# Optimization experiments

Hardware: AMD Instinct MI355X
Metric: run time of the kernel (lower is better)

Reference implementation:

```python
import jax, jax.numpy as jnp
import numpy as np
import math

B, S, D, H, DFF = 16, 512, 1024, 16, 4096
DK = D // H
EPS = 1e-6


def _lin(x, W, b):
    return x @ W + b


def _layernorm(x, g, b):
    # torch-style: unbiased std, eps added to std (not var)
    m = jnp.mean(x, axis=-1, keepdims=True)
    std = jnp.sqrt(jnp.sum((x - m) ** 2, axis=-1, keepdims=True) / (x.shape[-1] - 1))
    return g * (x - m) / (std + EPS) + b


def _gelu(x):
    return 0.5 * x * (1.0 + jnp.tanh(jnp.sqrt(2.0 / jnp.pi) * (x + 0.044715 * x ** 3)))


def setup_inputs() -> dict:
    key = jax.random.key(0)
    ks = jax.random.split(key, 20)
    sc = lambda fan_in: 1.0 / math.sqrt(fan_in)
    d = {
        "x": jax.random.normal(ks[0], (B, S, D), jnp.float32),
        "time": jax.random.normal(ks[1], (B, S, D), jnp.float32),
        "Wq": jax.random.uniform(ks[2], (D, D), jnp.float32, -sc(D), sc(D)),
        "bq": jnp.zeros((D,), jnp.float32),
        "Wk": jax.random.uniform(ks[3], (D, D), jnp.float32, -sc(D), sc(D)),
        "bk": jnp.zeros((D,), jnp.float32),
        "Wt": jax.random.uniform(ks[4], (D, D), jnp.float32, -sc(D), sc(D)),
        "bt": jnp.zeros((D,), jnp.float32),
        "Wv": jax.random.uniform(ks[5], (D, D), jnp.float32, -sc(D), sc(D)),
        "bv": jnp.zeros((D,), jnp.float32),
        "Wo": jax.random.uniform(ks[6], (D, D), jnp.float32, -sc(D), sc(D)),
        "bo": jnp.zeros((D,), jnp.float32),
        "W1": jax.random.uniform(ks[7], (D, DFF), jnp.float32, -sc(D), sc(D)),
        "b1": jnp.zeros((DFF,), jnp.float32),
        "W2": jax.random.uniform(ks[8], (DFF, D), jnp.float32, -sc(DFF), sc(DFF)),
        "b2": jnp.zeros((D,), jnp.float32),
        "ln1_g": jnp.ones((D,), jnp.float32),
        "ln1_b": jnp.zeros((D,), jnp.float32),
        "ln2_g": jnp.ones((D,), jnp.float32),
        "ln2_b": jnp.zeros((D,), jnp.float32),
        "mask_logits": jax.random.uniform(ks[9], (S, S), jnp.float32, 2.0, 5.0),
        "mask": jax.random.randint(ks[10], (B, 1, S, S), 0, 2, jnp.int32),
        "pmask": 0,
    }
    return d


def reference(x, time, Wq, bq, Wk, bk, Wt, bt, Wv, bv, Wo, bo, W1, b1, W2, b2,
              ln1_g, ln1_b, ln2_g, ln2_b, mask_logits, mask, pmask):
    def split_heads(t):  # [B,S,D] -> [B,H,S,DK]
        return t.reshape(B, S, H, DK).transpose(0, 2, 1, 3)

    # --- attention sublayer (dropout = identity at inference) ---
    xn = _layernorm(x, ln1_g, ln1_b)
    q = split_heads(_lin(xn, Wq, bq))
    k1 = split_heads(_lin(xn, Wk, bk))
    k2 = split_heads(_lin(time, Wt, bt))
    v = split_heads(_lin(xn, Wv, bv))

    inv = 1.0 / math.sqrt(DK)
    scores = jnp.einsum("bhqd,bhkd->bhqk", q, k1) * inv
    scores = jnp.where(mask == 0, -1e9, scores)  # masked_fill BEFORE time term
    scores = scores + jnp.einsum("bhqd,bhkd->bhqk", q, k2) * inv
    p_attn = jax.nn.softmax(scores, axis=-1)
    p_attn = p_attn * jax.nn.sigmoid(mask_logits)  # learned post-softmax mask [S,S]
    ctx = jnp.einsum("bhqk,bhkd->bhqd", p_attn, v)
    ctx = ctx.transpose(0, 2, 1, 3).reshape(B, S, D)
    x = x + _lin(ctx, Wo, bo)

    # --- FFN sublayer ---
    xn2 = _layernorm(x, ln2_g, ln2_b)
    ff = _lin(_gelu(_lin(xn2, W1, b1)), W2, b2)
    return x + ff
```

## Files before the change

### kernel.cpp

```cpp
#include <hip/hip_runtime.h>

#define BB   16
#define SS   512
#define DD   1024
#define HH   16
#define DKK  64
#define DFFN 4096
#define LN_EPS 1e-6f
#define QSCALE 0.18033688011112042f

typedef __attribute__((ext_vector_type(8))) __bf16 bf16x8;
typedef __attribute__((ext_vector_type(4))) float f32x4;
typedef __attribute__((ext_vector_type(8))) unsigned short ushort8;
typedef __attribute__((ext_vector_type(4))) unsigned short ushort4_t;

#define AS1 __attribute__((address_space(1)))
#define AS3 __attribute__((address_space(3)))

__device__ __forceinline__ unsigned short f2bf(float f) {
  unsigned int u = __float_as_uint(f);
  u += 0x7FFFu + ((u >> 16) & 1u);
  return (unsigned short)(u >> 16);
}
__device__ __forceinline__ float bf2f(unsigned short u) {
  return __uint_as_float(((unsigned int)u) << 16);
}

__device__ __forceinline__ float gelu_f(float x) {
  float x3 = x * x * x;
  return 0.5f * x * (1.0f + tanhf(0.7978845608028654f * (x + 0.044715f * x3)));
}

__device__ __forceinline__ void sbar() {
  __builtin_amdgcn_sched_barrier(0);
  __builtin_amdgcn_s_barrier();
  __builtin_amdgcn_sched_barrier(0);
}
#define WAITVM(N)                                         \
  do {                                                    \
    __builtin_amdgcn_sched_barrier(0);                    \
    asm volatile("s_waitcnt vmcnt(" #N ")" ::: "memory"); \
    __builtin_amdgcn_sched_barrier(0);                    \
  } while (0)

__global__ __launch_bounds__(256) void ln_kernel(const float* __restrict__ x,
                                                 const float* __restrict__ g,
                                                 const float* __restrict__ b,
                                                 unsigned short* __restrict__ out, int ldo) {
  const int row = blockIdx.x;
  const int tid = threadIdx.x;
  const float* xr = x + (size_t)row * DD;
  float4 v = *(const float4*)(xr + tid * 4);
  float s = v.x + v.y + v.z + v.w;
#pragma unroll
  for (int off = 1; off < 64; off <<= 1) s += __shfl_xor(s, off);
  __shared__ float red[8];
  const int wid = tid >> 6, l = tid & 63;
  if (l == 0) red[wid] = s;
  __syncthreads();
  const float mean = (red[0] + red[1] + red[2] + red[3]) * (1.0f / DD);
  float4 d;
  d.x = v.x - mean; d.y = v.y - mean; d.z = v.z - mean; d.w = v.w - mean;
  float ss = d.x * d.x + d.y * d.y + d.z * d.z + d.w * d.w;
#pragma unroll
  for (int off = 1; off < 64; off <<= 1) ss += __shfl_xor(ss, off);
  if (l == 0) red[4 + wid] = ss;
  __syncthreads();
  const float var = (red[4] + red[5] + red[6] + red[7]) * (1.0f / (DD - 1));
  const float scale = 1.0f / (sqrtf(var) + LN_EPS);
  float4 gv = *(const float4*)(g + tid * 4);
  float4 bv = *(const float4*)(b + tid * 4);
  ushort4_t o;
  o[0] = f2bf(gv.x * d.x * scale + bv.x);
  o[1] = f2bf(gv.y * d.y * scale + bv.y);
  o[2] = f2bf(gv.z * d.z * scale + bv.z);
  o[3] = f2bf(gv.w * d.w * scale + bv.w);
  *(ushort4_t*)(out + (size_t)row * ldo + tid * 4) = o;
}

__global__ __launch_bounds__(256) void cvt_bf16(const float* __restrict__ in,
                                                unsigned short* __restrict__ out, int ldo) {
  const int i = blockIdx.x * 256 + threadIdx.x;
  const int row = i >> 7;
  const int c0 = (i & 127) * 8;
  const float4* p = (const float4*)(in + (size_t)row * DD + c0);
  float4 a = p[0], b = p[1];
  ushort8 o;
  o[0] = f2bf(a.x); o[1] = f2bf(a.y); o[2] = f2bf(a.z); o[3] = f2bf(a.w);
  o[4] = f2bf(b.x); o[5] = f2bf(b.y); o[6] = f2bf(b.z); o[7] = f2bf(b.w);
  *(ushort8*)(out + (size_t)row * ldo + c0) = o;
}

__global__ __launch_bounds__(256) void transpose_cvt(const float* __restrict__ W,
                                                     unsigned short* __restrict__ WT,
                                                     int N, int ldo) {
  __shared__ float tile[32][33];
  const int tx = threadIdx.x & 31, ty = threadIdx.x >> 5;
  const int n0 = blockIdx.x * 32, k0 = blockIdx.y * 32;
#pragma unroll
  for (int i = 0; i < 32; i += 8)
    tile[ty + i][tx] = W[(size_t)(k0 + ty + i) * N + n0 + tx];
  __syncthreads();
#pragma unroll
  for (int i = 0; i < 32; i += 8)
    WT[(size_t)(n0 + ty + i) * ldo + k0 + tx] = f2bf(tile[tx][ty + i]);
}

__global__ __launch_bounds__(256) void vtrans(const unsigned short* __restrict__ in,
                                              unsigned short* __restrict__ out) {
  __shared__ unsigned short tile[64][72];
  const int t = threadIdx.x;
  const int c0 = blockIdx.x * 64;
  const int r0 = blockIdx.y * 64;
  const int tx = t & 15, ty = t >> 4;
#pragma unroll
  for (int i = 0; i < 64; i += 16)
    *(ushort4_t*)&tile[ty + i][tx * 4] =
        *(const ushort4_t*)(in + (size_t)(r0 + ty + i) * 1024 + c0 + tx * 4);
  __syncthreads();
  const int cT = t >> 2, rq = (t & 3) * 16;
  ushort8 o0, o1;
#pragma unroll
  for (int j = 0; j < 8; ++j) o0[j] = tile[rq + j][cT];
#pragma unroll
  for (int j = 0; j < 8; ++j) o1[j] = tile[rq + 8 + j][cT];
  *(ushort8*)(out + (size_t)(c0 + cT) * 8192 + r0 + rq) = o0;
  *(ushort8*)(out + (size_t)(c0 + cT) * 8192 + r0 + rq + 8) = o1;
}

__global__ __launch_bounds__(256) void bias_prep(const float* __restrict__ bq,
                                                 const float* __restrict__ bv,
                                                 const float* __restrict__ bk,
                                                 const float* __restrict__ bt,
                                                 float* __restrict__ qvb,
                                                 float* __restrict__ kcb) {
  const int i = blockIdx.x * 256 + threadIdx.x;
  if (i < 2048) qvb[i] = (i < 1024) ? bq[i] : bv[i - 1024];
  else kcb[i - 2048] = bk[i - 2048] + bt[i - 2048];
}

__global__ __launch_bounds__(256) void gate_build(const int* __restrict__ mask,
                                                  const float* __restrict__ ml,
                                                  unsigned short* __restrict__ gate) {
  const int i = blockIdx.x * 256 + threadIdx.x;
  const size_t base = (size_t)i * 8;
  const int off = (int)(base & (SS * SS - 1));
  const int4* mp = (const int4*)(mask + base);
  const int4 m0 = mp[0], m1 = mp[1];
  const float4* lp = (const float4*)(ml + off);
  const float4 a = lp[0], b = lp[1];
  ushort8 o;
  o[0] = m0.x ? f2bf(1.0f / (1.0f + __expf(-a.x))) : 0;
  o[1] = m0.y ? f2bf(1.0f / (1.0f + __expf(-a.y))) : 0;
  o[2] = m0.z ? f2bf(1.0f / (1.0f + __expf(-a.z))) : 0;
  o[3] = m0.w ? f2bf(1.0f / (1.0f + __expf(-a.w))) : 0;
  o[4] = m1.x ? f2bf(1.0f / (1.0f + __expf(-b.x))) : 0;
  o[5] = m1.y ? f2bf(1.0f / (1.0f + __expf(-b.y))) : 0;
  o[6] = m1.z ? f2bf(1.0f / (1.0f + __expf(-b.z))) : 0;
  o[7] = m1.w ? f2bf(1.0f / (1.0f + __expf(-b.w))) : 0;
  *(ushort8*)(gate + base) = o;
}

template <int BM, int EPI>
__global__ __launch_bounds__(512, 2) void gemm8p(const unsigned short* __restrict__ A, int lda,
                                                 const unsigned short* __restrict__ BT,
                                                 const float* __restrict__ bias,
                                                 const float* __restrict__ resid,
                                                 void* __restrict__ Cout,
                                                 unsigned short* __restrict__ vOut,
                                                 int M, int N, int K) {
  constexpr int MI = BM / 32;
  constexpr int ASUB = BM / 16;
  constexpr int AHALF = BM * 32;
  constexpr int ABUF = BM * 64;
  constexpr int ACALL = BM / 128;

  __shared__ __align__(16) unsigned short smA[2 * ABUF];
  __shared__ __align__(16) unsigned short smB[2 * 16384];

  const int tid = threadIdx.x;
  const int w = tid >> 6, lane = tid & 63;
  const int lr = lane & 15, lg = lane >> 4;
  const int wr = w >> 2, wn = w & 3;

  const int nb = N / 256;
  const int nwg = gridDim.x;
  int bid = blockIdx.x;
  bid = (bid & 7) * (nwg >> 3) + (bid >> 3);
  const int mb = bid / nb, nbk = bid % nb;

  const int uo = (lane * 16) ^ (lane & 32);
  const int srow = uo >> 6;
  const int scol = (uo & 63) >> 1;

  const unsigned short* pA[2];
  const unsigned short* pB[2];
#pragma unroll
  for (int j = 0; j < ACALL; ++j)
    pA[j] = A + (size_t)(mb * BM + (j * 8 + w) * 16 + srow) * lda + scol;
  if (ACALL == 1) pA[1] = pA[0];
#pragma unroll
  for (int j = 0; j < 2; ++j)
    pB[j] = BT + (size_t)(nbk * 256 + (j * 8 + w) * 16 + srow) * K + scol;

  auto stA = [&](int kt, int ks, int j, int d) {
    __builtin_amdgcn_global_load_lds(
        (const AS1 void*)(pA[j] + (size_t)kt * 64 + ks * 32),
        (AS3 void*)(smA + d * ABUF + ks * AHALF + j * 4096 + w * 512), 16, 0, 0);
  };
  auto stB = [&](int kt, int ks, int j, int d) {
    __builtin_amdgcn_global_load_lds(
        (const AS1 void*)(pB[j] + (size_t)kt * 64 + ks * 32),
        (AS3 void*)(smB + d * 16384 + ks * 8192 + j * 4096 + w * 512), 16, 0, 0);
  };

  const int aoff = lr * 32 + ((lg * 8) ^ ((lr & 8) << 1));

  f32x4 acc[MI][4] = {};
  const int NT = K >> 6;

#pragma unroll
  for (int j = 0; j < ACALL; ++j) stA(0, 0, j, 0);
  stB(0, 0, 0, 0); stB(0, 0, 1, 0);
#pragma unroll
  for (int j = 0; j < ACALL; ++j) stA(0, 1, j, 0);
  stB(0, 1, 0, 0); stB(0, 1, 1, 0);
  if constexpr (ACALL == 2) { WAITVM(4); } else { WAITVM(3); }
  sbar();

  for (int kt = 0; kt < NT; ++kt) {
    const unsigned short* aD = smA + (kt & 1) * ABUF;
    const unsigned short* bD = smB + (kt & 1) * 16384;
    const int dn = (kt & 1) ^ 1;
    const bool nx = (kt + 1 < NT);
    bf16x8 af[4], bf[4];

#pragma unroll
    for (int i = 0; i < 4; ++i)
      bf[i] = *(const bf16x8*)(bD + (wn * 4 + i) * 512 + aoff);
#pragma unroll
    for (int i = 0; i < 4; ++i)
      af[i] = *(const bf16x8*)(aD + (wr * MI + i) * 512 + aoff);
    if (nx) {
#pragma unroll
      for (int j = 0; j < ACALL; ++j) stA(kt + 1, 0, j, dn);
      if constexpr (ACALL == 1) { stB(kt + 1, 0, 0, dn); stB(kt + 1, 0, 1, dn); }
    }
    if constexpr (ACALL == 1) { WAITVM(3); }
    sbar();
    __builtin_amdgcn_s_setprio(1);
#pragma unroll
    for (int mi = 0; mi < 4; ++mi)
#pragma unroll
      for (int ni = 0; ni < 4; ++ni)
        acc[mi][ni] = __builtin_amdgcn_mfma_f32_16x16x32_bf16(af[mi], bf[ni], acc[mi][ni], 0, 0, 0);
    __builtin_amdgcn_s_setprio(0);
    sbar();

    if constexpr (ACALL == 2) {
#pragma unroll
      for (int i = 0; i < 4; ++i)
        af[i] = *(const bf16x8*)(aD + (wr * MI + 4 + i) * 512 + aoff);
      if (nx) { stB(kt + 1, 0, 0, dn); stB(kt + 1, 0, 1, dn); }
      WAITVM(4);
      sbar();
      __builtin_amdgcn_s_setprio(1);
#pragma unroll
      for (int mi = 0; mi < 4; ++mi)
#pragma unroll
        for (int ni = 0; ni < 4; ++ni)
          acc[4 + mi][ni] = __builtin_amdgcn_mfma_f32_16x16x32_bf16(af[mi], bf[ni], acc[4 + mi][ni], 0, 0, 0);
      __builtin_amdgcn_s_setprio(0);
      sbar();
    }

#pragma unroll
    for (int i = 0; i < 4; ++i)
      bf[i] = *(const bf16x8*)(bD + (16 + wn * 4 + i) * 512 + aoff);
#pragma unroll
    for (int i = 0; i < 4; ++i)
      af[i] = *(const bf16x8*)(aD + (ASUB + wr * MI + i) * 512 + aoff);
    if (nx) {
#pragma unroll
      for (int j = 0; j < ACALL; ++j) stA(kt + 1, 1, j, dn);
      if constexpr (ACALL == 1) { stB(kt + 1, 1, 0, dn); stB(kt + 1, 1, 1, dn); }
    }
    if constexpr (ACALL == 1) { WAITVM(3); }
    sbar();
    __builtin_amdgcn_s_setprio(1);
#pragma unroll
    for (int mi = 0; mi < 4; ++mi)
#pragma unroll
      for (int ni = 0; ni < 4; ++ni)
        acc[mi][ni] = __builtin_amdgcn_mfma_f32_16x16x32_bf16(af[mi], bf[ni], acc[mi][ni], 0, 0, 0);
    __builtin_amdgcn_s_setprio(0);
    sbar();

    if constexpr (ACALL == 2) {
#pragma unroll
      for (int i = 0; i < 4; ++i)
        af[i] = *(const bf16x8*)(aD + (ASUB + wr * MI + 4 + i) * 512 + aoff);
      if (nx) { stB(kt + 1, 1, 0, dn); stB(kt + 1, 1, 1, dn); }
      WAITVM(4);
      sbar();
      __builtin_amdgcn_s_setprio(1);
#pragma unroll
      for (int mi = 0; mi < 4; ++mi)
#pragma unroll
        for (int ni = 0; ni < 4; ++ni)
          acc[4 + mi][ni] = __builtin_amdgcn_mfma_f32_16x16x32_bf16(af[mi], bf[ni], acc[4 + mi][ni], 0, 0, 0);
      __builtin_amdgcn_s_setprio(0);
      sbar();
    }
  }

  const int colb = nbk * 256 + wn * 64;
  const int rowb = mb * BM + wr * (BM / 2);
#pragma unroll
  for (int ni = 0; ni < 4; ++ni) {
    const int col = colb + ni * 16 + lr;
    const float bv = bias[col];
#pragma unroll
    for (int mi = 0; mi < MI; ++mi) {
#pragma unroll
      for (int j = 0; j < 4; ++j) {
        const int row = rowb + mi * 16 + lg * 4 + j;
        float vv = acc[mi][ni][j] + bv;
        if (EPI == 2) vv = gelu_f(vv);
        if (EPI == 1) {
          const size_t o = (size_t)row * N + col;
          ((float*)Cout)[o] = vv + resid[o];
        } else if (EPI == 3) {
          if (colb >= 1024) {
            vOut[(size_t)row * 1024 + (col - 1024)] = f2bf(vv);
          } else {
            ((unsigned short*)Cout)[(size_t)row * 1024 + col] = f2bf(vv * QSCALE);
          }
        } else {
          ((unsigned short*)Cout)[(size_t)row * N + col] = f2bf(vv);
        }
      }
    }
  }
}

__global__ __launch_bounds__(256) void attn4(const unsigned short* __restrict__ qb,
                                             const unsigned short* __restrict__ vT,
                                             const unsigned short* __restrict__ kcb,
                                             const unsigned short* __restrict__ gate,
                                             unsigned short* __restrict__ ctx) {
  __shared__ __align__(16) unsigned char smem[33280];
  float* pctx = (float*)smem;
  float* sumw = (float*)(smem + 32768);

  const int tid = threadIdx.x;
  const int w = tid >> 6, l = tid & 63;
  const int lr = l & 15, lg = l >> 4;
  const int virt = (blockIdx.x & 7) * 512 + (blockIdx.x >> 3);
  const int qt = virt & 15;
  const int h = (virt >> 4) & 15;
  const int b = virt >> 8;
  const int q0 = qt * 32;

  const unsigned short* qg = qb + (size_t)b * SS * DD + h * DKK;
  const unsigned short* kg = kcb + (size_t)b * SS * DD + h * DKK;
  const unsigned short* vg = vT + (size_t)(h * DKK) * 8192 + b * SS;
  const unsigned short* gg = gate + (size_t)b * SS * SS;
  unsigned short* cg = ctx + (size_t)b * SS * DD + h * DKK;

  bf16x8 qf[2][2];
#pragma unroll
  for (int mi = 0; mi < 2; ++mi)
#pragma unroll
    for (int ks = 0; ks < 2; ++ks)
      qf[mi][ks] = *(const bf16x8*)(qg + (size_t)(q0 + mi * 16 + lr) * DD + ks * 32 + lg * 8);

  f32x4 acc[2][4] = {};
  float ssum[2][4] = {};
  const int kb0 = w * 128;

#pragma unroll
  for (int it = 0; it < 4; ++it) {
    const int kbase = kb0 + it * 32;
    unsigned short* Pb = (unsigned short*)smem + w * 2560 + (it & 1) * 1280;

    bf16x8 kf[2][2];
#pragma unroll
    for (int ni = 0; ni < 2; ++ni)
#pragma unroll
      for (int ks = 0; ks < 2; ++ks)
        kf[ni][ks] = *(const bf16x8*)(kg + (size_t)(kbase + ni * 16 + lr) * DD + ks * 32 + lg * 8);
    f32x4 sc[2][2] = {};
#pragma unroll
    for (int ks = 0; ks < 2; ++ks)
#pragma unroll
      for (int mi = 0; mi < 2; ++mi)
#pragma unroll
        for (int ni = 0; ni < 2; ++ni)
          sc[mi][ni] = __builtin_amdgcn_mfma_f32_16x16x32_bf16(qf[mi][ks], kf[ni][ks], sc[mi][ni], 0, 0, 0);

    bf16x8 vb[4];
#pragma unroll
    for (int dkg = 0; dkg < 4; ++dkg)
      vb[dkg] = *(const bf16x8*)(vg + (size_t)(dkg * 16 + lr) * 8192 + kbase + lg * 8);

#pragma unroll
    for (int mi = 0; mi < 2; ++mi)
#pragma unroll
      for (int ni = 0; ni < 2; ++ni)
#pragma unroll
        for (int j = 0; j < 4; ++j) {
          const int row = mi * 16 + lg * 4 + j;
          const unsigned short gu = gg[(size_t)(q0 + row) * SS + kbase + ni * 16 + lr];
          const float e = exp2f(sc[mi][ni][j]);
          ssum[mi][j] += gu ? e : 0.0f;
          Pb[row * 40 + ni * 16 + lr] = f2bf(e * bf2f(gu));
        }

#pragma unroll
    for (int mi = 0; mi < 2; ++mi) {
      const bf16x8 pa = *(const bf16x8*)(Pb + (mi * 16 + lr) * 40 + lg * 8);
#pragma unroll
      for (int dkg = 0; dkg < 4; ++dkg)
        acc[mi][dkg] = __builtin_amdgcn_mfma_f32_16x16x32_bf16(pa, vb[dkg], acc[mi][dkg], 0, 0, 0);
    }
  }

#pragma unroll
  for (int mi = 0; mi < 2; ++mi)
#pragma unroll
    for (int j = 0; j < 4; ++j) {
      float s = ssum[mi][j];
      s += __shfl_xor(s, 1);
      s += __shfl_xor(s, 2);
      s += __shfl_xor(s, 4);
      s += __shfl_xor(s, 8);
      if (lr == 0) sumw[w * 32 + mi * 16 + lg * 4 + j] = s;
    }
  __syncthreads();

#pragma unroll
  for (int mi = 0; mi < 2; ++mi)
#pragma unroll
    for (int dkg = 0; dkg < 4; ++dkg)
#pragma unroll
      for (int j = 0; j < 4; ++j)
        pctx[(size_t)w * 2048 + (mi * 16 + lg * 4 + j) * 64 + dkg * 16 + lr] = acc[mi][dkg][j];
  __syncthreads();

  {
    const int row = tid >> 3;
    const int dk0 = (tid & 7) * 8;
    const float tot = sumw[row] + sumw[32 + row] + sumw[64 + row] + sumw[96 + row];
    const float inv = 1.0f / fmaxf(tot, 1e-30f);
    float vsum[8];
#pragma unroll
    for (int c = 0; c < 8; ++c) vsum[c] = 0.0f;
#pragma unroll
    for (int ww = 0; ww < 4; ++ww) {
      const float* p = pctx + (size_t)ww * 2048 + row * 64 + dk0;
      f32x4 a = *(const f32x4*)p;
      f32x4 bq = *(const f32x4*)(p + 4);
#pragma unroll
      for (int c = 0; c < 4; ++c) { vsum[c] += a[c]; vsum[4 + c] += bq[c]; }
    }
    ushort8 o;
#pragma unroll
    for (int c = 0; c < 8; ++c) o[c] = f2bf(vsum[c] * inv);
    *(ushort8*)(cg + (size_t)(q0 + row) * DD + dk0) = o;
  }
}

extern "C" void kernel_launch(void* const* d_in, const int* in_sizes, int n_in,
                              void* d_out, int out_size, void* d_ws, size_t ws_size,
                              hipStream_t stream) {
  (void)in_sizes; (void)n_in; (void)out_size; (void)ws_size;
  const float* x    = (const float*)d_in[0];
  const float* timep= (const float*)d_in[1];
  const float* Wq = (const float*)d_in[2];  const float* bq = (const float*)d_in[3];
  const float* Wk = (const float*)d_in[4];  const float* bk = (const float*)d_in[5];
  const float* Wt = (const float*)d_in[6];  const float* bt = (const float*)d_in[7];
  const float* Wv = (const float*)d_in[8];  const float* bv = (const float*)d_in[9];
  const float* Wo = (const float*)d_in[10]; const float* bo = (const float*)d_in[11];
  const float* W1 = (const float*)d_in[12]; const float* b1 = (const float*)d_in[13];
  const float* W2 = (const float*)d_in[14]; const float* b2 = (const float*)d_in[15];
  const float* ln1g = (const float*)d_in[16]; const float* ln1b = (const float*)d_in[17];
  const float* ln2g = (const float*)d_in[18]; const float* ln2b = (const float*)d_in[19];
  const float* ml   = (const float*)d_in[20];
  const int*   mask = (const int*)d_in[21];
  float* out = (float*)d_out;

  char* w = (char*)d_ws;
  auto alloc = [&](size_t sz) { char* p = w; w += (sz + 255) & ~(size_t)255; return p; };
  const int MT = BB * SS;

  unsigned short* WqvT = (unsigned short*)alloc((size_t)2048 * 1024 * 2);
  unsigned short* WkcT = (unsigned short*)alloc((size_t)1024 * 2048 * 2);
  unsigned short* WoT  = (unsigned short*)alloc((size_t)DD * DD * 2);
  unsigned short* W1T  = (unsigned short*)alloc((size_t)DD * DFFN * 2);
  unsigned short* W2T  = (unsigned short*)alloc((size_t)DFFN * DD * 2);
  float* qvb = (float*)alloc(2048 * 4);
  float* kcbias = (float*)alloc(1024 * 4);
  unsigned short* gateb = (unsigned short*)alloc((size_t)BB * SS * SS * 2);
  unsigned short* xt2 = (unsigned short*)alloc((size_t)MT * 2048 * 2);
  unsigned short* qbuf = (unsigned short*)alloc((size_t)MT * DD * 2);
  unsigned short* vbuf = (unsigned short*)alloc((size_t)MT * DD * 2);
  unsigned short* vTb = (unsigned short*)alloc((size_t)DD * MT * 2);
  unsigned short* kcb = (unsigned short*)alloc((size_t)MT * DD * 2);
  float*          x2  = (float*)alloc((size_t)MT * DD * 4);
  unsigned short* hb  = (unsigned short*)alloc((size_t)MT * DFFN * 2);
  unsigned short* ctx = xt2;
  unsigned short* xn2 = xt2;

  transpose_cvt<<<dim3(32, 32), 256, 0, stream>>>(Wq, WqvT, 1024, 1024);
  transpose_cvt<<<dim3(32, 32), 256, 0, stream>>>(Wv, WqvT + (size_t)1024 * 1024, 1024, 1024);
  transpose_cvt<<<dim3(32, 32), 256, 0, stream>>>(Wk, WkcT, 1024, 2048);
  transpose_cvt<<<dim3(32, 32), 256, 0, stream>>>(Wt, WkcT + 1024, 1024, 2048);
  transpose_cvt<<<dim3(32, 32), 256, 0, stream>>>(Wo, WoT, 1024, 1024);
  transpose_cvt<<<dim3(128, 32), 256, 0, stream>>>(W1, W1T, 4096, 1024);
  transpose_cvt<<<dim3(32, 128), 256, 0, stream>>>(W2, W2T, 1024, 4096);
  bias_prep<<<dim3(12), 256, 0, stream>>>(bq, bv, bk, bt, qvb, kcbias);
  gate_build<<<dim3(BB * SS * SS / 8 / 256), 256, 0, stream>>>(mask, ml, gateb);

  ln_kernel<<<dim3(MT), 256, 0, stream>>>(x, ln1g, ln1b, xt2, 2048);
  cvt_bf16<<<dim3(MT * DD / 8 / 256), 256, 0, stream>>>(timep, xt2 + 1024, 2048);

  gemm8p<256, 3><<<dim3(256), 512, 0, stream>>>(xt2, 2048, WqvT, qvb, nullptr, (void*)qbuf, vbuf, MT, 2048, 1024);
  vtrans<<<dim3(16, 128), 256, 0, stream>>>(vbuf, vTb);
  gemm8p<128, 0><<<dim3(256), 512, 0, stream>>>(xt2, 2048, WkcT, kcbias, nullptr, (void*)kcb, nullptr, MT, 1024, 2048);

  attn4<<<dim3(BB * HH * 16), 256, 0, stream>>>(qbuf, vTb, kcb, gateb, ctx);

  gemm8p<128, 1><<<dim3(256), 512, 0, stream>>>(ctx, 1024, WoT, bo, x, (void*)x2, nullptr, MT, 1024, 1024);
  ln_kernel<<<dim3(MT), 256, 0, stream>>>(x2, ln2g, ln2b, xn2, 1024);
  gemm8p<256, 2><<<dim3(512), 512, 0, stream>>>(xn2, 1024, W1T, b1, nullptr, (void*)hb, nullptr, MT, 4096, 1024);
  gemm8p<128, 1><<<dim3(256), 512, 0, stream>>>(hb, 4096, W2T, b2, x2, (void*)out, nullptr, MT, 1024, 4096);
}
```

Measured before the change: 518.0 us.

## Deepen GEMM prefetch to half-tile granularity and restructure epilogue loops

The GEMM main loop now issues global-to-LDS loads one half-tile further ahead: the second half of tile k+1 and the first half of tile k+2 are prefetched during tile k. Wait counts are adjusted so more loads stay in flight. This aims to hide global memory latency better. The epilogue is also reordered so bias loads are hoisted and the V-output branch is handled separately, which may improve store coalescing per row. Deeper prefetch into the double buffer risks overwriting LDS still being read if the barrier and wait ordering is wrong.

```diff
diff --git a/kernel.cpp b/kernel.cpp
--- a/kernel.cpp
+++ b/kernel.cpp
@@ -213,26 +213,30 @@
         (const AS1 void*)(pB[j] + (size_t)kt * 64 + ks * 32),
         (AS3 void*)(smB + d * 16384 + ks * 8192 + j * 4096 + w * 512), 16, 0, 0);
   };
+  auto issue_half = [&](int t, int ks) {
+    const int d = t & 1;
+#pragma unroll
+    for (int j = 0; j < ACALL; ++j) stA(t, ks, j, d);
+    stB(t, ks, 0, d);
+    stB(t, ks, 1, d);
+  };
 
   const int aoff = lr * 32 + ((lg * 8) ^ ((lr & 8) << 1));
 
   f32x4 acc[MI][4] = {};
   const int NT = K >> 6;
 
-#pragma unroll
-  for (int j = 0; j < ACALL; ++j) stA(0, 0, j, 0);
-  stB(0, 0, 0, 0); stB(0, 0, 1, 0);
-#pragma unroll
-  for (int j = 0; j < ACALL; ++j) stA(0, 1, j, 0);
-  stB(0, 1, 0, 0); stB(0, 1, 1, 0);
-  if constexpr (ACALL == 2) { WAITVM(4); } else { WAITVM(3); }
+  issue_half(0, 0);
+  issue_half(0, 1);
+  issue_half(1, 0);
+  if constexpr (ACALL == 2) { WAITVM(8); } else { WAITVM(6); }
   sbar();
 
   for (int kt = 0; kt < NT; ++kt) {
     const unsigned short* aD = smA + (kt & 1) * ABUF;
     const unsigned short* bD = smB + (kt & 1) * 16384;
-    const int dn = (kt & 1) ^ 1;
-    const bool nx = (kt + 1 < NT);
+    const bool i1 = (kt + 1 < NT);
+    const bool i2 = (kt + 2 < NT);
     bf16x8 af[4], bf[4];
 
 #pragma unroll
@@ -241,12 +245,10 @@
 #pragma unroll
     for (int i = 0; i < 4; ++i)
       af[i] = *(const bf16x8*)(aD + (wr * MI + i) * 512 + aoff);
-    if (nx) {
-#pragma unroll
-      for (int j = 0; j < ACALL; ++j) stA(kt + 1, 0, j, dn);
-      if constexpr (ACALL == 1) { stB(kt + 1, 0, 0, dn); stB(kt + 1, 0, 1, dn); }
-    }
-    if constexpr (ACALL == 1) { WAITVM(3); }
+    if (i1) issue_half(kt + 1, 1);
+    if constexpr (ACALL == 1) {
+      if (i1) { WAITVM(6); } else { WAITVM(0); }
+    }
     sbar();
     __builtin_amdgcn_s_setprio(1);
 #pragma unroll
@@ -261,8 +263,7 @@
 #pragma unroll
       for (int i = 0; i < 4; ++i)
         af[i] = *(const bf16x8*)(aD + (wr * MI + 4 + i) * 512 + aoff);
-      if (nx) { stB(kt + 1, 0, 0, dn); stB(kt + 1, 0, 1, dn); }
-      WAITVM(4);
+      if (i1) { WAITVM(8); } else { WAITVM(0); }
       sbar();
       __builtin_amdgcn_s_setprio(1);
 #pragma unroll
@@ -280,12 +281,10 @@
 #pragma unroll
     for (int i = 0; i < 4; ++i)
       af[i] = *(const bf16x8*)(aD + (ASUB + wr * MI + i) * 512 + aoff);
-    if (nx) {
-#pragma unroll
-      for (int j = 0; j < ACALL; ++j) stA(kt + 1, 1, j, dn);
-      if constexpr (ACALL == 1) { stB(kt + 1, 1, 0, dn); stB(kt + 1, 1, 1, dn); }
-    }
-    if constexpr (ACALL == 1) { WAITVM(3); }
+    if (i2) issue_half(kt + 2, 0);
+    if constexpr (ACALL == 1) {
+      if (i2) { WAITVM(6); } else { WAITVM(3); }
+    }
     sbar();
     __builtin_amdgcn_s_setprio(1);
 #pragma unroll
@@ -300,8 +299,7 @@
 #pragma unroll
       for (int i = 0; i < 4; ++i)
         af[i] = *(const bf16x8*)(aD + (ASUB + wr * MI + 4 + i) * 512 + aoff);
-      if (nx) { stB(kt + 1, 1, 0, dn); stB(kt + 1, 1, 1, dn); }
-      WAITVM(4);
+      if (i2) { WAITVM(8); } else { WAITVM(4); }
       sbar();
       __builtin_amdgcn_s_setprio(1);
 #pragma unroll
@@ -316,28 +314,40 @@
 
   const int colb = nbk * 256 + wn * 64;
   const int rowb = mb * BM + wr * (BM / 2);
-#pragma unroll
-  for (int ni = 0; ni < 4; ++ni) {
-    const int col = colb + ni * 16 + lr;
-    const float bv = bias[col];
+  float bvv[4];
+#pragma unroll
+  for (int ni = 0; ni < 4; ++ni) bvv[ni] = bias[colb + ni * 16 + lr];
+
+  if (EPI == 3 && colb >= 1024) {
 #pragma unroll
     for (int mi = 0; mi < MI; ++mi) {
 #pragma unroll
       for (int j = 0; j < 4; ++j) {
         const int row = rowb + mi * 16 + lg * 4 + j;
-        float vv = acc[mi][ni][j] + bv;
-        if (EPI == 2) vv = gelu_f(vv);
-        if (EPI == 1) {
-          const size_t o = (size_t)row * N + col;
-          ((float*)Cout)[o] = vv + resid[o];
-        } else if (EPI == 3) {
-          if (colb >= 1024) {
-            vOut[(size_t)row * 1024 + (col - 1024)] = f2bf(vv);
+#pragma unroll
+        for (int ni = 0; ni < 4; ++ni)
+          vOut[(size_t)row * 1024 + (colb - 1024) + ni * 16 + lr] = f2bf(acc[mi][ni][j] + bvv[ni]);
+      }
+    }
+  } else {
+#pragma unroll
+    for (int mi = 0; mi < MI; ++mi) {
+#pragma unroll
+      for (int j = 0; j < 4; ++j) {
+        const int row = rowb + mi * 16 + lg * 4 + j;
+#pragma unroll
+        for (int ni = 0; ni < 4; ++ni) {
+          const int col = colb + ni * 16 + lr;
+          float vv = acc[mi][ni][j] + bvv[ni];
+          if (EPI == 2) vv = gelu_f(vv);
+          if (EPI == 1) {
+            const size_t o = (size_t)row * N + col;
+            ((float*)Cout)[o] = vv + resid[o];
+          } else if (EPI == 3) {
+            ((unsigned short*)Cout)[(size_t)row * 1024 + col] = f2bf(vv * QSCALE);
           } else {
-            ((unsigned short*)Cout)[(size_t)row * 1024 + col] = f2bf(vv * QSCALE);
+            ((unsigned short*)Cout)[(size_t)row * N + col] = f2bf(vv);
           }
-        } else {
-          ((unsigned short*)Cout)[(size_t)row * N + col] = f2bf(vv);
         }
       }
     }
```

Measured after the change: 487.3 us. -5.9%, faster.
